# Kernel tuning notes

Hardware: AMD Instinct MI355X
Metric: run time of the kernel (lower is better)

The kernel has to match this reference:

```python
import jax, jax.numpy as jnp
import numpy as np

D = 32        # number of TT cores (d)
R = 16        # tt_rank
B = 262144    # batch size


def setup_inputs() -> dict:
    key = jax.random.key(0)
    k1, k2, k3, k4 = jax.random.split(key, 4)
    return {
        "X": jax.random.randint(k1, (B, D), 0, 2, dtype=jnp.int32),
        "core_first": jax.random.normal(k2, (1, R, 2), dtype=jnp.float32),
        "cores_mid": jax.random.normal(k3, (D - 2, R, R, 2), dtype=jnp.float32),
        "core_last": jax.random.normal(k4, (R, 1, 2), dtype=jnp.float32),
    }


def reference(X, core_first, cores_mid, core_last):
    # First core: cores[0][:, :, X[:,0]] -> [1, R, B] -> permute -> [B, 1, R].
    # We carry the squeezed [B, R] row vector instead of [B, 1, R].
    carry0 = jnp.take(core_first[0], X[:, 0], axis=-1).T  # [B, R]

    def step(carry, inp):
        core, idx = inp                       # core: [R, R, 2], idx: [B]
        c = jnp.take(core, idx, axis=2)       # gathered core: [R, R, B]
        new = jnp.einsum('br,rsb->bs', carry, c)  # batched (1xR)@(RxR)
        return new, None

    # Middle cores i = 1 .. D-2 (sequential chain, data-dependent).
    carry, _ = jax.lax.scan(step, carry0, (cores_mid, X[:, 1:D - 1].T))

    # Last core: cores[-1][:, :, X[:,-1]] -> [R, 1, B]; contract to scalar per batch.
    c_last = jnp.take(core_last[:, 0, :], X[:, -1], axis=-1)  # [R, B]
    out = jnp.einsum('br,rb->b', carry, c_last)               # [B]  (squeeze of [B,1,1])
    return out
```

## Files before the change

kernel.cpp:

```cpp
#include <hip/hip_runtime.h>


#define R 16
#define TT_D 32
#define BATCH 262144

#define OFF_V4   0
#define OFF_A    256
#define OFF_B    (256 + 1*4096)
#define OFF_C    (256 + 2*4096)
#define OFF_Dm   (256 + 3*4096)
#define OFF_E    (256 + 4*4096)
#define OFF_F    (256 + 5*4096)
#define OFF_W4   (256 + 6*4096)
#define OFF_V8   (OFF_W4 + 256)
#define OFF_P8   (OFF_V8 + 4096)
#define OFF_Q8   (OFF_P8 + 65536)
#define OFF_W8   (OFF_Q8 + 65536)
#define OFF_V16  (OFF_W8 + 4096)
#define OFF_W16  (OFF_V16 + 1048576)
#define WS_FLOATS (OFF_W16 + 1048576)

__global__ __launch_bounds__(256) void tt_nibble(const float* __restrict__ cf,
                                                 const float* __restrict__ cm,
                                                 const float* __restrict__ cl,
                                                 float* __restrict__ ws) {
    const int tbl = blockIdx.x;
    const int t = threadIdx.x;

    if (tbl >= 1 && tbl <= 6) {
        const int e = t >> 4, r = t & 15;
        const int base = 3 + (tbl - 1) * 4;
        const int b0 = (e >> 3) & 1, b1 = (e >> 2) & 1, b2 = (e >> 1) & 1, b3 = e & 1;
        float v[R], nv[R];
        const float* M0 = cm + base * 512;
        #pragma unroll
        for (int s2 = 0; s2 < R; s2++) v[s2] = M0[(r * 16 + s2) * 2 + b0];
        const int bits[3] = { b1, b2, b3 };
        for (int k = 1; k <= 3; k++) {
            const float* M = cm + (base + k) * 512;
            const int bb = bits[k - 1];
            #pragma unroll
            for (int s2 = 0; s2 < R; s2++) {
                float acc = 0.f;
                #pragma unroll
                for (int tt = 0; tt < R; tt++) acc += v[tt] * M[(tt * 16 + s2) * 2 + bb];
                nv[s2] = acc;
            }
            #pragma unroll
            for (int s2 = 0; s2 < R; s2++) v[s2] = nv[s2];
        }
        float* o = ws + OFF_A + (tbl - 1) * 4096 + e * 256 + r * 16;
        #pragma unroll
        for (int s2 = 0; s2 < R; s2++) o[s2] = v[s2];
    } else if (tbl == 0) {
        if (t < 16) {
            const int e = t;
            const int b0 = (e >> 3) & 1, b1 = (e >> 2) & 1, b2 = (e >> 1) & 1, b3 = e & 1;
            float v[R], nv[R];
            #pragma unroll
            for (int s2 = 0; s2 < R; s2++) v[s2] = cf[s2 * 2 + b0];
            const int bits[3] = { b1, b2, b3 };
            for (int k = 1; k <= 3; k++) {
                const float* M = cm + (k - 1) * 512;
                const int bb = bits[k - 1];
                #pragma unroll
                for (int s2 = 0; s2 < R; s2++) {
                    float acc = 0.f;
                    #pragma unroll
                    for (int tt = 0; tt < R; tt++) acc += v[tt] * M[(tt * 16 + s2) * 2 + bb];
                    nv[s2] = acc;
                }
                #pragma unroll
                for (int s2 = 0; s2 < R; s2++) v[s2] = nv[s2];
            }
            float* o = ws + OFF_V4 + e * 16;
            #pragma unroll
            for (int s2 = 0; s2 < R; s2++) o[s2] = v[s2];
        }
    } else {
        if (t < 16) {
            const int e = t;
            const int b0 = (e >> 3) & 1, b1 = (e >> 2) & 1, b2 = (e >> 1) & 1, b3 = e & 1;
            float w[R], nw[R];
            #pragma unroll
            for (int r2 = 0; r2 < R; r2++) w[r2] = cl[r2 * 2 + b3];
            const int cores[3] = { 29, 28, 27 };
            const int bits[3] = { b2, b1, b0 };
            for (int k = 0; k < 3; k++) {
                const float* M = cm + cores[k] * 512;
                const int bb = bits[k];
                #pragma unroll
                for (int r2 = 0; r2 < R; r2++) {
                    float acc = 0.f;
                    #pragma unroll
                    for (int tt = 0; tt < R; tt++) acc += M[(r2 * 16 + tt) * 2 + bb] * w[tt];
                    nw[r2] = acc;
                }
                #pragma unroll
                for (int r2 = 0; r2 < R; r2++) w[r2] = nw[r2];
            }
            float* o = ws + OFF_W4 + e * 16;
            #pragma unroll
            for (int r2 = 0; r2 < R; r2++) o[r2] = w[r2];
        }
    }
}

__global__ __launch_bounds__(256) void tt_byte(float* __restrict__ ws) {
    const int g = blockIdx.x;
    const int t = threadIdx.x;
    if (g < 32) {
        const bool isP = (g < 16);
        const int idx = (isP ? g : g - 16) * 256 + t;
        const int e = idx >> 4, r = idx & 15;
        const int h = e >> 4, l = e & 15;
        const float* Hm = ws + (isP ? OFF_B : OFF_Dm) + h * 256;
        const float* Lm = ws + (isP ? OFF_C : OFF_E) + l * 256;
        float hrow[R];
        #pragma unroll
        for (int k = 0; k < R; k++) hrow[k] = Hm[r * 16 + k];
        float outv[R];
        #pragma unroll
        for (int s2 = 0; s2 < R; s2++) outv[s2] = 0.f;
        #pragma unroll
        for (int k = 0; k < R; k++) {
            const float a = hrow[k];
            #pragma unroll
            for (int s2 = 0; s2 < R; s2++) outv[s2] += a * Lm[k * 16 + s2];
        }
        float* o = ws + (isP ? OFF_P8 : OFF_Q8) + e * 256 + r * 16;
        #pragma unroll
        for (int s2 = 0; s2 < R; s2++) o[s2] = outv[s2];
    } else if (g == 32) {
        const int e = t, h = e >> 4, l = e & 15;
        const float* v4 = ws + OFF_V4 + h * 16;
        const float* Am = ws + OFF_A + l * 256;
        float outv[R];
        #pragma unroll
        for (int s2 = 0; s2 < R; s2++) outv[s2] = 0.f;
        #pragma unroll
        for (int k = 0; k < R; k++) {
            const float a = v4[k];
            #pragma unroll
            for (int s2 = 0; s2 < R; s2++) outv[s2] += a * Am[k * 16 + s2];
        }
        float* o = ws + OFF_V8 + e * 16;
        #pragma unroll
        for (int s2 = 0; s2 < R; s2++) o[s2] = outv[s2];
    } else {
        const int e = t, h = e >> 4, l = e & 15;
        const float* Fm = ws + OFF_F + h * 256;
        const float* w4 = ws + OFF_W4 + l * 16;
        float outv[R];
        #pragma unroll
        for (int r2 = 0; r2 < R; r2++) {
            float acc = 0.f;
            #pragma unroll
            for (int k = 0; k < R; k++) acc += Fm[r2 * 16 + k] * w4[k];
            outv[r2] = acc;
        }
        float* o = ws + OFF_W8 + e * 16;
        #pragma unroll
        for (int r2 = 0; r2 < R; r2++) o[r2] = outv[r2];
    }
}

__global__ __launch_bounds__(256) void tt_final(float* __restrict__ ws) {
    const int t = threadIdx.x;
    if (blockIdx.x < 256) {
        const int h = blockIdx.x, l = t;
        __shared__ float sv[16];
        if (t < 16) sv[t] = ws[OFF_V8 + h * 16 + t];
        __syncthreads();
        const float* P = ws + OFF_P8 + l * 256;
        float outv[R];
        #pragma unroll
        for (int s2 = 0; s2 < R; s2++) outv[s2] = 0.f;
        #pragma unroll
        for (int r2 = 0; r2 < R; r2++) {
            const float a = sv[r2];
            #pragma unroll
            for (int s2 = 0; s2 < R; s2++) outv[s2] += a * P[r2 * 16 + s2];
        }
        float* o = ws + OFF_V16 + (size_t)(h * 256 + l) * 16;
        #pragma unroll
        for (int s2 = 0; s2 < R; s2++) o[s2] = outv[s2];
    } else {
        const int h = blockIdx.x - 256, l = t;
        __shared__ float sQ[256];
        sQ[t] = ws[OFF_Q8 + h * 256 + t];
        __syncthreads();
        const float* wv = ws + OFF_W8 + l * 16;
        float w[R];
        #pragma unroll
        for (int k = 0; k < R; k++) w[k] = wv[k];
        float outv[R];
        #pragma unroll
        for (int r2 = 0; r2 < R; r2++) {
            float acc = 0.f;
            #pragma unroll
            for (int k = 0; k < R; k++) acc += sQ[r2 * 16 + k] * w[k];
            outv[r2] = acc;
        }
        float* o = ws + OFF_W16 + (size_t)(h * 256 + l) * 16;
        #pragma unroll
        for (int r2 = 0; r2 < R; r2++) o[r2] = outv[r2];
    }
}

__global__ __launch_bounds__(256) void tt_main(const int* __restrict__ X,
                                               const float* __restrict__ ws,
                                               float* __restrict__ out) {
    const int b = blockIdx.x * 256 + threadIdx.x;
    const int4* Xr = (const int4*)(X + (size_t)b * TT_D);
    int xv[TT_D];
    #pragma unroll
    for (int q = 0; q < 8; q++) {
        int4 c = Xr[q];
        xv[q * 4 + 0] = c.x; xv[q * 4 + 1] = c.y; xv[q * 4 + 2] = c.z; xv[q * 4 + 3] = c.w;
    }
    unsigned p = 0, s = 0;
    #pragma unroll
    for (int i = 0; i < 16; i++) p = (p << 1) | (unsigned)(xv[i] & 1);
    #pragma unroll
    for (int i = 16; i < 32; i++) s = (s << 1) | (unsigned)(xv[i] & 1);

    const float4* v = (const float4*)(ws + OFF_V16 + (size_t)p * 16);
    const float4* w = (const float4*)(ws + OFF_W16 + (size_t)s * 16);
    float acc = 0.f;
    #pragma unroll
    for (int k = 0; k < 4; k++) {
        float4 a = v[k], c = w[k];
        acc += a.x * c.x + a.y * c.y + a.z * c.z + a.w * c.w;
    }
    out[b] = acc;
}

__global__ __launch_bounds__(256) void tt_direct(const int* __restrict__ X,
                                                 const float* __restrict__ cf,
                                                 const float* __restrict__ cm,
                                                 const float* __restrict__ cl,
                                                 float* __restrict__ out) {
    __shared__ float scm[30 * 16 * 16 * 2];
    for (int i = threadIdx.x; i < 30 * 16 * 16 * 2; i += blockDim.x) scm[i] = cm[i];
    __syncthreads();
    const int b = blockIdx.x * blockDim.x + threadIdx.x;
    if (b >= BATCH) return;
    const int* xr = X + (size_t)b * TT_D;
    float v[R], nv[R];
    const int x0 = xr[0] & 1;
    #pragma unroll
    for (int r = 0; r < R; r++) v[r] = cf[r * 2 + x0];
    for (int i = 1; i <= 30; i++) {
        const int bit = xr[i] & 1;
        const float* M = scm + (i - 1) * 512;
        #pragma unroll
        for (int s2 = 0; s2 < R; s2++) {
            float acc = 0.f;
            #pragma unroll
            for (int r = 0; r < R; r++) acc += v[r] * M[(r * 16 + s2) * 2 + bit];
            nv[s2] = acc;
        }
        #pragma unroll
        for (int s2 = 0; s2 < R; s2++) v[s2] = nv[s2];
    }
    const int xl = xr[31] & 1;
    float acc = 0.f;
    #pragma unroll
    for (int r = 0; r < R; r++) acc += v[r] * cl[r * 2 + xl];
    out[b] = acc;
}

extern "C" void kernel_launch(void* const* d_in, const int* in_sizes, int n_in,
                              void* d_out, int out_size, void* d_ws, size_t ws_size,
                              hipStream_t stream) {
    const int* X = (const int*)d_in[0];
    const float* cf = (const float*)d_in[1];
    const float* cm = (const float*)d_in[2];
    const float* cl = (const float*)d_in[3];
    float* out = (float*)d_out;

    if (ws_size >= (size_t)WS_FLOATS * sizeof(float)) {
        float* ws = (float*)d_ws;
        tt_nibble<<<8, 256, 0, stream>>>(cf, cm, cl, ws);
        tt_byte<<<34, 256, 0, stream>>>(ws);
        tt_final<<<512, 256, 0, stream>>>(ws);
        tt_main<<<BATCH / 256, 256, 0, stream>>>(X, ws, out);
    } else {
        tt_direct<<<(BATCH + 255) / 256, 256, 0, stream>>>(X, cf, cm, cl, out);
    }
}
```

Before: 123.0 us.

## Fuse three table-building kernels into one redundant-compute build kernel

Replaces the three precompute launches (nibble, byte and final table builds) with a single 512-block kernel. Each block recomputes the small 4-core chain tables it needs in shared memory (padded strides to avoid bank conflicts) and writes its slice of the 16-bit prefix/suffix tables directly. This removes two launch boundaries and the global-memory round trips for the intermediate tables. In exchange every block redundantly recomputes several 4-core chains, which adds arithmetic and needs roughly 35 KB of shared memory per block, lowering occupancy.

```diff
diff --git a/kernel.cpp b/kernel.cpp
--- a/kernel.cpp
+++ b/kernel.cpp
@@ -5,207 +5,188 @@
 #define TT_D 32
 #define BATCH 262144
 
-#define OFF_V4   0
-#define OFF_A    256
-#define OFF_B    (256 + 1*4096)
-#define OFF_C    (256 + 2*4096)
-#define OFF_Dm   (256 + 3*4096)
-#define OFF_E    (256 + 4*4096)
-#define OFF_F    (256 + 5*4096)
-#define OFF_W4   (256 + 6*4096)
-#define OFF_V8   (OFF_W4 + 256)
-#define OFF_P8   (OFF_V8 + 4096)
-#define OFF_Q8   (OFF_P8 + 65536)
-#define OFF_W8   (OFF_Q8 + 65536)
-#define OFF_V16  (OFF_W8 + 4096)
-#define OFF_W16  (OFF_V16 + 1048576)
-#define WS_FLOATS (OFF_W16 + 1048576)
-
-__global__ __launch_bounds__(256) void tt_nibble(const float* __restrict__ cf,
-                                                 const float* __restrict__ cm,
-                                                 const float* __restrict__ cl,
-                                                 float* __restrict__ ws) {
-    const int tbl = blockIdx.x;
+#define OFF_V16  0
+#define OFF_W16  1048576
+#define WS_FLOATS 2097152
+
+#define MSTRIDE 268
+#define VSTRIDE 17
+
+__device__ __forceinline__ void row_chain4(const float* __restrict__ cm, int base,
+                                           int e, int r, float* __restrict__ out) {
+    const int b0 = (e >> 3) & 1, b1 = (e >> 2) & 1, b2 = (e >> 1) & 1, b3 = e & 1;
+    float v[R], nv[R];
+    const float* M0 = cm + base * 512;
+    #pragma unroll
+    for (int s = 0; s < R; s++) v[s] = M0[(r * 16 + s) * 2 + b0];
+    const int bits[3] = { b1, b2, b3 };
+    #pragma unroll
+    for (int k = 1; k <= 3; k++) {
+        const float* M = cm + (base + k) * 512;
+        const int bb = bits[k - 1];
+        #pragma unroll
+        for (int s = 0; s < R; s++) {
+            float a = 0.f;
+            #pragma unroll
+            for (int t2 = 0; t2 < R; t2++) a += v[t2] * M[(t2 * 16 + s) * 2 + bb];
+            nv[s] = a;
+        }
+        #pragma unroll
+        for (int s = 0; s < R; s++) v[s] = nv[s];
+    }
+    #pragma unroll
+    for (int s = 0; s < R; s++) out[s] = v[s];
+}
+
+__global__ __launch_bounds__(256) void tt_build(const float* __restrict__ cf,
+                                                const float* __restrict__ cm,
+                                                const float* __restrict__ cl,
+                                                float* __restrict__ ws) {
+    __shared__ float T0[16 * MSTRIDE];
+    __shared__ float T1[16 * MSTRIDE];
+    __shared__ float SA[16 * VSTRIDE];
+    __shared__ float SE[16 * VSTRIDE];
+    __shared__ float SV[32];
+    __shared__ float SG[256];
+
     const int t = threadIdx.x;
-
-    if (tbl >= 1 && tbl <= 6) {
-        const int e = t >> 4, r = t & 15;
-        const int base = 3 + (tbl - 1) * 4;
-        const int b0 = (e >> 3) & 1, b1 = (e >> 2) & 1, b2 = (e >> 1) & 1, b3 = e & 1;
-        float v[R], nv[R];
-        const float* M0 = cm + base * 512;
-        #pragma unroll
-        for (int s2 = 0; s2 < R; s2++) v[s2] = M0[(r * 16 + s2) * 2 + b0];
-        const int bits[3] = { b1, b2, b3 };
-        for (int k = 1; k <= 3; k++) {
-            const float* M = cm + (base + k) * 512;
-            const int bb = bits[k - 1];
-            #pragma unroll
-            for (int s2 = 0; s2 < R; s2++) {
-                float acc = 0.f;
-                #pragma unroll
-                for (int tt = 0; tt < R; tt++) acc += v[tt] * M[(tt * 16 + s2) * 2 + bb];
-                nv[s2] = acc;
+    const int e = t >> 4, r = t & 15;
+    float tmp[R];
+
+    if (blockIdx.x < 256) {
+        const int h = blockIdx.x;
+        row_chain4(cm, 7, e, r, tmp);
+        #pragma unroll
+        for (int s = 0; s < R; s++) T0[e * MSTRIDE + r * 16 + s] = tmp[s];
+        row_chain4(cm, 11, e, r, tmp);
+        #pragma unroll
+        for (int s = 0; s < R; s++) T1[e * MSTRIDE + r * 16 + s] = tmp[s];
+        if (t < 16) {
+            row_chain4(cm, 3, h & 15, t, tmp);
+            #pragma unroll
+            for (int s = 0; s < R; s++) SA[t * VSTRIDE + s] = tmp[s];
+        } else if (t == 16) {
+            const int n0 = h >> 4;
+            const int b0 = (n0 >> 3) & 1, b1 = (n0 >> 2) & 1, b2 = (n0 >> 1) & 1, b3 = n0 & 1;
+            float v[R], nv[R];
+            #pragma unroll
+            for (int s = 0; s < R; s++) v[s] = cf[s * 2 + b0];
+            const int bits[3] = { b1, b2, b3 };
+            #pragma unroll
+            for (int k = 0; k < 3; k++) {
+                const float* M = cm + k * 512;
+                const int bb = bits[k];
+                #pragma unroll
+                for (int s = 0; s < R; s++) {
+                    float a = 0.f;
+                    #pragma unroll
+                    for (int t2 = 0; t2 < R; t2++) a += v[t2] * M[(t2 * 16 + s) * 2 + bb];
+                    nv[s] = a;
+                }
+                #pragma unroll
+                for (int s = 0; s < R; s++) v[s] = nv[s];
             }
             #pragma unroll
-            for (int s2 = 0; s2 < R; s2++) v[s2] = nv[s2];
-        }
-        float* o = ws + OFF_A + (tbl - 1) * 4096 + e * 256 + r * 16;
-        #pragma unroll
-        for (int s2 = 0; s2 < R; s2++) o[s2] = v[s2];
-    } else if (tbl == 0) {
+            for (int s = 0; s < R; s++) SV[s] = v[s];
+        }
+        __syncthreads();
         if (t < 16) {
-            const int e = t;
-            const int b0 = (e >> 3) & 1, b1 = (e >> 2) & 1, b2 = (e >> 1) & 1, b3 = e & 1;
-            float v[R], nv[R];
-            #pragma unroll
-            for (int s2 = 0; s2 < R; s2++) v[s2] = cf[s2 * 2 + b0];
-            const int bits[3] = { b1, b2, b3 };
-            for (int k = 1; k <= 3; k++) {
-                const float* M = cm + (k - 1) * 512;
-                const int bb = bits[k - 1];
-                #pragma unroll
-                for (int s2 = 0; s2 < R; s2++) {
-                    float acc = 0.f;
-                    #pragma unroll
-                    for (int tt = 0; tt < R; tt++) acc += v[tt] * M[(tt * 16 + s2) * 2 + bb];
-                    nv[s2] = acc;
-                }
-                #pragma unroll
-                for (int s2 = 0; s2 < R; s2++) v[s2] = nv[s2];
-            }
-            float* o = ws + OFF_V4 + e * 16;
-            #pragma unroll
-            for (int s2 = 0; s2 < R; s2++) o[s2] = v[s2];
-        }
+            float a = 0.f;
+            #pragma unroll
+            for (int k = 0; k < R; k++) a += SV[k] * SA[k * VSTRIDE + t];
+            SV[16 + t] = a;
+        }
+        __syncthreads();
+        const float* Bm = T0 + (t >> 4) * MSTRIDE;
+        const float* Cm = T1 + (t & 15) * MSTRIDE;
+        float u1[R];
+        #pragma unroll
+        for (int s = 0; s < R; s++) u1[s] = 0.f;
+        #pragma unroll
+        for (int k = 0; k < R; k++) {
+            const float a = SV[16 + k];
+            #pragma unroll
+            for (int s = 0; s < R; s++) u1[s] += a * Bm[k * 16 + s];
+        }
+        float u2[R];
+        #pragma unroll
+        for (int s = 0; s < R; s++) u2[s] = 0.f;
+        #pragma unroll
+        for (int k = 0; k < R; k++) {
+            const float a = u1[k];
+            #pragma unroll
+            for (int s = 0; s < R; s++) u2[s] += a * Cm[k * 16 + s];
+        }
+        float* o = ws + OFF_V16 + (size_t)(h * 256 + t) * 16;
+        #pragma unroll
+        for (int s = 0; s < R; s++) o[s] = u2[s];
     } else {
+        const int h = blockIdx.x - 256;
+        row_chain4(cm, 23, e, r, tmp);
+        #pragma unroll
+        for (int s = 0; s < R; s++) T0[e * MSTRIDE + r * 16 + s] = tmp[s];
         if (t < 16) {
-            const int e = t;
-            const int b0 = (e >> 3) & 1, b1 = (e >> 2) & 1, b2 = (e >> 1) & 1, b3 = e & 1;
+            const int b0 = (t >> 3) & 1, b1 = (t >> 2) & 1, b2 = (t >> 1) & 1, b3 = t & 1;
             float w[R], nw[R];
             #pragma unroll
             for (int r2 = 0; r2 < R; r2++) w[r2] = cl[r2 * 2 + b3];
             const int cores[3] = { 29, 28, 27 };
             const int bits[3] = { b2, b1, b0 };
+            #pragma unroll
             for (int k = 0; k < 3; k++) {
                 const float* M = cm + cores[k] * 512;
                 const int bb = bits[k];
                 #pragma unroll
                 for (int r2 = 0; r2 < R; r2++) {
-                    float acc = 0.f;
+                    float a = 0.f;
                     #pragma unroll
-                    for (int tt = 0; tt < R; tt++) acc += M[(r2 * 16 + tt) * 2 + bb] * w[tt];
-                    nw[r2] = acc;
+                    for (int t2 = 0; t2 < R; t2++) a += M[(r2 * 16 + t2) * 2 + bb] * w[t2];
+                    nw[r2] = a;
                 }
                 #pragma unroll
                 for (int r2 = 0; r2 < R; r2++) w[r2] = nw[r2];
             }
-            float* o = ws + OFF_W4 + e * 16;
-            #pragma unroll
-            for (int r2 = 0; r2 < R; r2++) o[r2] = w[r2];
-        }
-    }
-}
-
-__global__ __launch_bounds__(256) void tt_byte(float* __restrict__ ws) {
-    const int g = blockIdx.x;
-    const int t = threadIdx.x;
-    if (g < 32) {
-        const bool isP = (g < 16);
-        const int idx = (isP ? g : g - 16) * 256 + t;
-        const int e = idx >> 4, r = idx & 15;
-        const int h = e >> 4, l = e & 15;
-        const float* Hm = ws + (isP ? OFF_B : OFF_Dm) + h * 256;
-        const float* Lm = ws + (isP ? OFF_C : OFF_E) + l * 256;
-        float hrow[R];
-        #pragma unroll
-        for (int k = 0; k < R; k++) hrow[k] = Hm[r * 16 + k];
-        float outv[R];
-        #pragma unroll
-        for (int s2 = 0; s2 < R; s2++) outv[s2] = 0.f;
-        #pragma unroll
-        for (int k = 0; k < R; k++) {
-            const float a = hrow[k];
-            #pragma unroll
-            for (int s2 = 0; s2 < R; s2++) outv[s2] += a * Lm[k * 16 + s2];
-        }
-        float* o = ws + (isP ? OFF_P8 : OFF_Q8) + e * 256 + r * 16;
-        #pragma unroll
-        for (int s2 = 0; s2 < R; s2++) o[s2] = outv[s2];
-    } else if (g == 32) {
-        const int e = t, h = e >> 4, l = e & 15;
-        const float* v4 = ws + OFF_V4 + h * 16;
-        const float* Am = ws + OFF_A + l * 256;
-        float outv[R];
-        #pragma unroll
-        for (int s2 = 0; s2 < R; s2++) outv[s2] = 0.f;
-        #pragma unroll
-        for (int k = 0; k < R; k++) {
-            const float a = v4[k];
-            #pragma unroll
-            for (int s2 = 0; s2 < R; s2++) outv[s2] += a * Am[k * 16 + s2];
-        }
-        float* o = ws + OFF_V8 + e * 16;
-        #pragma unroll
-        for (int s2 = 0; s2 < R; s2++) o[s2] = outv[s2];
-    } else {
-        const int e = t, h = e >> 4, l = e & 15;
-        const float* Fm = ws + OFF_F + h * 256;
-        const float* w4 = ws + OFF_W4 + l * 16;
-        float outv[R];
+            #pragma unroll
+            for (int r2 = 0; r2 < R; r2++) T1[t * VSTRIDE + r2] = w[r2];
+        } else if (t >= 64 && t < 80) {
+            row_chain4(cm, 15, h >> 4, t - 64, tmp);
+            #pragma unroll
+            for (int s = 0; s < R; s++) SA[(t - 64) * VSTRIDE + s] = tmp[s];
+        } else if (t >= 80 && t < 96) {
+            row_chain4(cm, 19, h & 15, t - 80, tmp);
+            #pragma unroll
+            for (int s = 0; s < R; s++) SE[(t - 80) * VSTRIDE + s] = tmp[s];
+        }
+        __syncthreads();
+        {
+            const int gr = t >> 4, gc = t & 15;
+            float a = 0.f;
+            #pragma unroll
+            for (int k = 0; k < R; k++) a += SA[gr * VSTRIDE + k] * SE[k * VSTRIDE + gc];
+            SG[t] = a;
+        }
+        __syncthreads();
+        const float* Fm = T0 + (t >> 4) * MSTRIDE;
+        const float* w4 = T1 + (t & 15) * VSTRIDE;
+        float w[R];
         #pragma unroll
         for (int r2 = 0; r2 < R; r2++) {
-            float acc = 0.f;
-            #pragma unroll
-            for (int k = 0; k < R; k++) acc += Fm[r2 * 16 + k] * w4[k];
-            outv[r2] = acc;
-        }
-        float* o = ws + OFF_W8 + e * 16;
-        #pragma unroll
-        for (int r2 = 0; r2 < R; r2++) o[r2] = outv[r2];
-    }
-}
-
-__global__ __launch_bounds__(256) void tt_final(float* __restrict__ ws) {
-    const int t = threadIdx.x;
-    if (blockIdx.x < 256) {
-        const int h = blockIdx.x, l = t;
-        __shared__ float sv[16];
-        if (t < 16) sv[t] = ws[OFF_V8 + h * 16 + t];
-        __syncthreads();
-        const float* P = ws + OFF_P8 + l * 256;
-        float outv[R];
-        #pragma unroll
-        for (int s2 = 0; s2 < R; s2++) outv[s2] = 0.f;
+            float a = 0.f;
+            #pragma unroll
+            for (int k = 0; k < R; k++) a += Fm[r2 * 16 + k] * w4[k];
+            w[r2] = a;
+        }
+        float o2[R];
         #pragma unroll
         for (int r2 = 0; r2 < R; r2++) {
-            const float a = sv[r2];
-            #pragma unroll
-            for (int s2 = 0; s2 < R; s2++) outv[s2] += a * P[r2 * 16 + s2];
-        }
-        float* o = ws + OFF_V16 + (size_t)(h * 256 + l) * 16;
-        #pragma unroll
-        for (int s2 = 0; s2 < R; s2++) o[s2] = outv[s2];
-    } else {
-        const int h = blockIdx.x - 256, l = t;
-        __shared__ float sQ[256];
-        sQ[t] = ws[OFF_Q8 + h * 256 + t];
-        __syncthreads();
-        const float* wv = ws + OFF_W8 + l * 16;
-        float w[R];
-        #pragma unroll
-        for (int k = 0; k < R; k++) w[k] = wv[k];
-        float outv[R];
-        #pragma unroll
-        for (int r2 = 0; r2 < R; r2++) {
-            float acc = 0.f;
-            #pragma unroll
-            for (int k = 0; k < R; k++) acc += sQ[r2 * 16 + k] * w[k];
-            outv[r2] = acc;
-        }
-        float* o = ws + OFF_W16 + (size_t)(h * 256 + l) * 16;
-        #pragma unroll
-        for (int r2 = 0; r2 < R; r2++) o[r2] = outv[r2];
+            float a = 0.f;
+            #pragma unroll
+            for (int c = 0; c < R; c++) a += SG[r2 * 16 + c] * w[c];
+            o2[r2] = a;
+        }
+        float* o = ws + OFF_W16 + (size_t)(h * 256 + t) * 16;
+        #pragma unroll
+        for (int r2 = 0; r2 < R; r2++) o[r2] = o2[r2];
     }
 }
 
@@ -283,9 +264,7 @@
 
     if (ws_size >= (size_t)WS_FLOATS * sizeof(float)) {
         float* ws = (float*)d_ws;
-        tt_nibble<<<8, 256, 0, stream>>>(cf, cm, cl, ws);
-        tt_byte<<<34, 256, 0, stream>>>(ws);
-        tt_final<<<512, 256, 0, stream>>>(ws);
+        tt_build<<<512, 256, 0, stream>>>(cf, cm, cl, ws);
         tt_main<<<BATCH / 256, 256, 0, stream>>>(X, ws, out);
     } else {
         tt_direct<<<(BATCH + 255) / 256, 256, 0, stream>>>(X, cf, cm, cl, out);
```

Result: slower. 198.0 us (+60.9%).
